# Kernel tuning notes

Hardware: AMD Instinct MI355X
Metric: run time of the kernel (lower is better)

## Reference

```python
import jax, jax.numpy as jnp
import numpy as np

ALPHA = 1.0
LAMBDA_ADV = 0.5
MARGIN = 0.5
EPS = 1e-8  # torch F.cosine_similarity eps


def setup_inputs() -> dict:
    key = jax.random.key(0)
    k1, k2, k3 = jax.random.split(key, 3)
    B, D, C = 8192, 1024, 1000
    features = jax.random.normal(k1, (B, D), dtype=jnp.float32)
    labels = jax.random.randint(k2, (B,), 0, C, dtype=jnp.int64)
    centers = jax.random.normal(k3, (C, D), dtype=jnp.float32)
    return {"features": features, "labels": labels, "centers": centers}


def reference(features, labels, centers):
    # --- intra-class term: gather centers, cosine-decayed MSE ---
    cb = centers[labels]                                   # [B, D]
    f_norm = jnp.maximum(jnp.linalg.norm(features, axis=1), EPS)   # [B]
    c_norm = jnp.maximum(jnp.linalg.norm(cb, axis=1), EPS)         # [B]
    sim = jnp.sum(features * cb, axis=1) / (f_norm * c_norm)       # [B]
    sq_err = jnp.sum((features - cb) ** 2, axis=1)                 # [B]
    intra_loss = jnp.mean(sq_err / jnp.exp(ALPHA * sim))

    # --- adversarial term: pairwise cosine sim as normalize + GEMM ---
    fhat = features / f_norm[:, None]                       # [B, D]
    sim_matrix = fhat @ fhat.T                              # [B, B]
    mask = labels[:, None] != labels[None, :]               # [B, B] bool
    hinge = jnp.where(mask, jax.nn.relu(MARGIN - sim_matrix), 0.0)
    n_pairs = jnp.maximum(jnp.sum(mask), 1).astype(hinge.dtype)
    adv_loss = jnp.sum(hinge) / n_pairs

    return intra_loss + LAMBDA_ADV * adv_loss
```

## Files before the change

### kernel.cpp

```cpp
#include <hip/hip_runtime.h>


typedef __attribute__((ext_vector_type(8))) short bf16x8;
typedef __attribute__((ext_vector_type(4))) float f32x4;

#define NROWS 8192
#define NDIM  1024
#define NCLS  1000
#define NTILE 32
#define NTRI  528

#define FHAT_OFF  0
#define INTRA_OFF 16777216
#define ADV_OFF   (INTRA_OFF + NROWS * 4)
#define HIST_OFF  (ADV_OFF + NTRI * 4)
#define WS_NEEDED (HIST_OFF + NCLS * 4)

static __device__ __forceinline__ unsigned short f2bf(float x) {
  unsigned u = __float_as_uint(x);
  u += 0x7fffu + ((u >> 16) & 1u);
  return (unsigned short)(u >> 16);
}

__global__ __launch_bounds__(256) void prep_kernel(
    const float* __restrict__ feat, const int* __restrict__ labels,
    const float* __restrict__ centers, unsigned short* __restrict__ fhat,
    float* __restrict__ intra_val, int* __restrict__ hist) {
  const int tid = threadIdx.x, wave = tid >> 6, lane = tid & 63;
  const int row = blockIdx.x * 4 + wave;

  const float4* fr = (const float4*)(feat + (size_t)row * NDIM);
  const int lab = labels[row];
  const float4* cr = (const float4*)(centers + (size_t)lab * NDIM);

  float4 f[4], c[4];
  #pragma unroll
  for (int j = 0; j < 4; ++j) { f[j] = fr[lane + j * 64]; c[j] = cr[lane + j * 64]; }

  float ff = 0.f, fc = 0.f, cc = 0.f, se = 0.f;
  #pragma unroll
  for (int j = 0; j < 4; ++j) {
    ff += f[j].x*f[j].x + f[j].y*f[j].y + f[j].z*f[j].z + f[j].w*f[j].w;
    fc += f[j].x*c[j].x + f[j].y*c[j].y + f[j].z*c[j].z + f[j].w*c[j].w;
    cc += c[j].x*c[j].x + c[j].y*c[j].y + c[j].z*c[j].z + c[j].w*c[j].w;
    float dx = f[j].x-c[j].x, dy = f[j].y-c[j].y, dz = f[j].z-c[j].z, dw = f[j].w-c[j].w;
    se += dx*dx + dy*dy + dz*dz + dw*dw;
  }

  #pragma unroll
  for (int off = 1; off < 64; off <<= 1) {
    ff += __shfl_xor(ff, off, 64);
    fc += __shfl_xor(fc, off, 64);
    cc += __shfl_xor(cc, off, 64);
    se += __shfl_xor(se, off, 64);
  }

  const float fn = fmaxf(sqrtf(ff), 1e-8f);
  const float cn = fmaxf(sqrtf(cc), 1e-8f);
  const float inv = 1.0f / fn;
  if (lane == 0) {
    intra_val[row] = se * expf(-(fc / (fn * cn)));
    atomicAdd(&hist[lab], 1);
  }

  ushort4* orow = (ushort4*)(fhat + (size_t)row * NDIM);
  #pragma unroll
  for (int j = 0; j < 4; ++j) {
    ushort4 o;
    o.x = f2bf(f[j].x * inv); o.y = f2bf(f[j].y * inv);
    o.z = f2bf(f[j].z * inv); o.w = f2bf(f[j].w * inv);
    orow[lane + j * 64] = o;
  }
}

#define CUMUL(r) ((r) * NTILE - (r) * ((r) - 1) / 2)

__global__ __launch_bounds__(512) void gemm_hinge_kernel(
    const unsigned short* __restrict__ fhat, const int* __restrict__ labels,
    float* __restrict__ adv_val) {
  const int bid0 = blockIdx.x;
  const int bid  = (bid0 & 7) * 66 + (bid0 >> 3);
  const float nf = (float)NTILE + 0.5f;
  int ti = (int)floorf(nf - sqrtf(nf * nf - 2.0f * (float)bid));
  while (ti > 0 && bid < CUMUL(ti)) --ti;
  while (bid >= CUMUL(ti + 1)) ++ti;
  const int tj = ti + (bid - CUMUL(ti));

  __shared__ __align__(16) unsigned short Al[2][256 * 32];
  __shared__ __align__(16) unsigned short Bl[2][256 * 32];
  __shared__ int labi[256], labj[256];
  __shared__ float rsum[8];

  const int tid  = threadIdx.x;
  const int wave = tid >> 6, lane = tid & 63;
  const int wr = wave >> 2, wc = wave & 3;

  if (tid < 256) labi[tid] = labels[ti * 256 + tid];
  else           labj[tid - 256] = labels[tj * 256 + (tid - 256)];

  f32x4 acc[8][4] = {};

  const int srow = tid >> 2;
  const int scol = (tid & 3) * 8;
  const unsigned short* a0 = fhat + (size_t)(ti * 256 + srow) * NDIM + scol;
  const unsigned short* b0 = fhat + (size_t)(tj * 256 + srow) * NDIM + scol;

#define STAGE(buf, k0)                                                        \
  do {                                                                        \
    _Pragma("unroll")                                                         \
    for (int l = 0; l < 2; ++l) {                                             \
      __builtin_amdgcn_global_load_lds(                                       \
          (const __attribute__((address_space(1))) void*)(a0 + (k0) +         \
              (size_t)l * 128 * NDIM),                                        \
          (__attribute__((address_space(3))) void*)&Al[buf][l * 4096 + wave * 512], \
          16, 0, 0);                                                          \
      __builtin_amdgcn_global_load_lds(                                       \
          (const __attribute__((address_space(1))) void*)(b0 + (k0) +         \
              (size_t)l * 128 * NDIM),                                        \
          (__attribute__((address_space(3))) void*)&Bl[buf][l * 4096 + wave * 512], \
          16, 0, 0);                                                          \
    }                                                                         \
  } while (0)

#define COMPUTE(buf)                                                          \
  do {                                                                        \
    const int lr = lane & 15;                                                 \
    const int lk = (lane >> 4) * 8;                                           \
    bf16x8 a[8], b[4];                                                        \
    _Pragma("unroll")                                                         \
    for (int m = 0; m < 8; ++m)                                               \
      a[m] = *(const bf16x8*)&Al[buf][(wr * 128 + m * 16 + lr) * 32 + lk];    \
    _Pragma("unroll")                                                         \
    for (int n = 0; n < 4; ++n)                                               \
      b[n] = *(const bf16x8*)&Bl[buf][(wc * 64 + n * 16 + lr) * 32 + lk];     \
    _Pragma("unroll")                                                         \
    for (int m = 0; m < 8; ++m)                                               \
      _Pragma("unroll")                                                       \
      for (int n = 0; n < 4; ++n)                                             \
        acc[m][n] = __builtin_amdgcn_mfma_f32_16x16x32_bf16(                  \
            a[m], b[n], acc[m][n], 0, 0, 0);                                  \
  } while (0)

  STAGE(0, 0);
  __syncthreads();
  for (int t = 0; t < 31; ++t) {
    const int cur = t & 1;
    STAGE(cur ^ 1, (t + 1) * 32);
    COMPUTE(cur);
    __syncthreads();
  }
  COMPUTE(1);

#undef STAGE
#undef COMPUTE

  float hs = 0.f;
  const int crow = (lane >> 4) * 4;
  const int ccol = lane & 15;
  #pragma unroll
  for (int m = 0; m < 8; ++m) {
    #pragma unroll
    for (int n = 0; n < 4; ++n) {
      #pragma unroll
      for (int r = 0; r < 4; ++r) {
        const int i = wr * 128 + m * 16 + crow + r;
        const int j = wc * 64 + n * 16 + ccol;
        if (labi[i] != labj[j]) {
          hs += fmaxf(0.5f - acc[m][n][r], 0.f);
        }
      }
    }
  }
  #pragma unroll
  for (int off = 32; off; off >>= 1) hs += __shfl_down(hs, off, 64);
  if (lane == 0) rsum[wave] = hs;
  __syncthreads();
  if (tid == 0) {
    float s = 0.f;
    #pragma unroll
    for (int w = 0; w < 8; ++w) s += rsum[w];
    if (ti != tj) s *= 2.f;
    adv_val[bid0] = s;
  }
}

__global__ __launch_bounds__(1024) void finalize_kernel(
    const float* __restrict__ intra_val, const float* __restrict__ adv_val,
    const int* __restrict__ hist, float* __restrict__ out) {
  __shared__ float rsi[16], rsa[16];
  __shared__ long long rsq[16];
  const int tid = threadIdx.x;
  const int wave = tid >> 6, lane = tid & 63;

  float si = 0.f;
  for (int i = tid; i < NROWS; i += 1024) si += intra_val[i];
  float sa = 0.f;
  if (tid < NTRI) sa = adv_val[tid];
  long long sq = 0;
  if (tid < NCLS) { long long h = hist[tid]; sq = h * h; }

  #pragma unroll
  for (int off = 32; off; off >>= 1) {
    si += __shfl_down(si, off, 64);
    sa += __shfl_down(sa, off, 64);
    sq += __shfl_down(sq, off, 64);
  }
  if (lane == 0) { rsi[wave] = si; rsa[wave] = sa; rsq[wave] = sq; }
  __syncthreads();
  if (tid == 0) {
    float SI = 0.f, SA = 0.f; long long SQ = 0;
    for (int w = 0; w < 16; ++w) { SI += rsi[w]; SA += rsa[w]; SQ += rsq[w]; }
    long long npairs = (long long)NROWS * NROWS - SQ;
    if (npairs < 1) npairs = 1;
    out[0] = SI / (float)NROWS + 0.5f * (SA / (float)npairs);
  }
}

__global__ void sentinel_kernel(float* out) {
  if (threadIdx.x == 0 && blockIdx.x == 0) out[0] = -1.0f;
}

extern "C" void kernel_launch(void* const* d_in, const int* in_sizes, int n_in,
                              void* d_out, int out_size, void* d_ws, size_t ws_size,
                              hipStream_t stream) {
  const float* feat    = (const float*)d_in[0];
  const int*   labels  = (const int*)d_in[1];
  const float* centers = (const float*)d_in[2];
  float* out = (float*)d_out;

  if (ws_size < (size_t)WS_NEEDED) {
    sentinel_kernel<<<1, 64, 0, stream>>>(out);
    return;
  }

  char* ws = (char*)d_ws;
  unsigned short* fhat = (unsigned short*)(ws + FHAT_OFF);
  float* intra_val = (float*)(ws + INTRA_OFF);
  float* adv_val   = (float*)(ws + ADV_OFF);
  int*   hist      = (int*)(ws + HIST_OFF);

  hipMemsetAsync(ws + HIST_OFF, 0, NCLS * 4, stream);

  prep_kernel<<<NROWS / 4, 256, 0, stream>>>(feat, labels, centers, fhat,
                                             intra_val, hist);
  gemm_hinge_kernel<<<NTRI, 512, 0, stream>>>(fhat, labels, adv_val);
  finalize_kernel<<<1, 1024, 0, stream>>>(intra_val, adv_val, hist, out);
}
```

Baseline: 204.9 us.

## Double K-tile to 64 with XOR-swizzled LDS and explicit waitcnt pipelining

Result: faster. 182.0 us (-11.2%).

```diff
diff --git a/kernel.cpp b/kernel.cpp
--- a/kernel.cpp
+++ b/kernel.cpp
@@ -46,7 +46,6 @@
     float dx = f[j].x-c[j].x, dy = f[j].y-c[j].y, dz = f[j].z-c[j].z, dw = f[j].w-c[j].w;
     se += dx*dx + dy*dy + dz*dz + dw*dw;
   }
-
   #pragma unroll
   for (int off = 1; off < 64; off <<= 1) {
     ff += __shfl_xor(ff, off, 64);
@@ -54,7 +53,6 @@
     cc += __shfl_xor(cc, off, 64);
     se += __shfl_xor(se, off, 64);
   }
-
   const float fn = fmaxf(sqrtf(ff), 1e-8f);
   const float cn = fmaxf(sqrtf(cc), 1e-8f);
   const float inv = 1.0f / fn;
@@ -62,7 +60,6 @@
     intra_val[row] = se * expf(-(fc / (fn * cn)));
     atomicAdd(&hist[lab], 1);
   }
-
   ushort4* orow = (ushort4*)(fhat + (size_t)row * NDIM);
   #pragma unroll
   for (int j = 0; j < 4; ++j) {
@@ -86,8 +83,8 @@
   while (bid >= CUMUL(ti + 1)) ++ti;
   const int tj = ti + (bid - CUMUL(ti));
 
-  __shared__ __align__(16) unsigned short Al[2][256 * 32];
-  __shared__ __align__(16) unsigned short Bl[2][256 * 32];
+  __shared__ __align__(16) unsigned short Al[2][256 * 64];
+  __shared__ __align__(16) unsigned short Bl[2][256 * 64];
   __shared__ int labi[256], labj[256];
   __shared__ float rsum[8];
 
@@ -100,57 +97,81 @@
 
   f32x4 acc[8][4] = {};
 
-  const int srow = tid >> 2;
-  const int scol = (tid & 3) * 8;
-  const unsigned short* a0 = fhat + (size_t)(ti * 256 + srow) * NDIM + scol;
-  const unsigned short* b0 = fhat + (size_t)(tj * 256 + srow) * NDIM + scol;
-
-#define STAGE(buf, k0)                                                        \
+  const int l8 = lane >> 3;
+  const int sl = ((lane & 7) ^ l8) * 8;
+  const unsigned short* aS = fhat + (size_t)(ti * 256 + wave * 32 + l8) * NDIM + sl;
+  const unsigned short* bS = fhat + (size_t)(tj * 256 + wave * 32 + l8) * NDIM + sl;
+
+#define STAGE(BUF, K0)                                                        \
   do {                                                                        \
     _Pragma("unroll")                                                         \
-    for (int l = 0; l < 2; ++l) {                                             \
+    for (int j = 0; j < 4; ++j) {                                             \
       __builtin_amdgcn_global_load_lds(                                       \
-          (const __attribute__((address_space(1))) void*)(a0 + (k0) +         \
-              (size_t)l * 128 * NDIM),                                        \
-          (__attribute__((address_space(3))) void*)&Al[buf][l * 4096 + wave * 512], \
+          (const __attribute__((address_space(1))) void*)(aS + (K0) + j * 8 * NDIM), \
+          (__attribute__((address_space(3))) void*)&Al[BUF][(wave * 4 + j) * 512],   \
           16, 0, 0);                                                          \
       __builtin_amdgcn_global_load_lds(                                       \
-          (const __attribute__((address_space(1))) void*)(b0 + (k0) +         \
-              (size_t)l * 128 * NDIM),                                        \
-          (__attribute__((address_space(3))) void*)&Bl[buf][l * 4096 + wave * 512], \
+          (const __attribute__((address_space(1))) void*)(bS + (K0) + j * 8 * NDIM), \
+          (__attribute__((address_space(3))) void*)&Bl[BUF][(wave * 4 + j) * 512],   \
           16, 0, 0);                                                          \
     }                                                                         \
   } while (0)
 
-#define COMPUTE(buf)                                                          \
+  const int lr = lane & 15;
+  const int hk = (lane >> 4) * 8;
+  const int xr = (lr & 7) << 3;
+
+#define COMPUTE(BUF)                                                          \
   do {                                                                        \
-    const int lr = lane & 15;                                                 \
-    const int lk = (lane >> 4) * 8;                                           \
-    bf16x8 a[8], b[4];                                                        \
     _Pragma("unroll")                                                         \
-    for (int m = 0; m < 8; ++m)                                               \
-      a[m] = *(const bf16x8*)&Al[buf][(wr * 128 + m * 16 + lr) * 32 + lk];    \
-    _Pragma("unroll")                                                         \
-    for (int n = 0; n < 4; ++n)                                               \
-      b[n] = *(const bf16x8*)&Bl[buf][(wc * 64 + n * 16 + lr) * 32 + lk];     \
-    _Pragma("unroll")                                                         \
-    for (int m = 0; m < 8; ++m)                                               \
+    for (int kk = 0; kk < 2; ++kk) {                                          \
+      const int lk = kk * 32 + hk;                                            \
+      const int lx = lk ^ xr;                                                 \
+      bf16x8 a[8], b[4];                                                      \
+      _Pragma("unroll")                                                       \
+      for (int m = 0; m < 8; ++m)                                             \
+        a[m] = *(const bf16x8*)&Al[BUF][(wr * 128 + m * 16 + lr) * 64 + lx];  \
       _Pragma("unroll")                                                       \
       for (int n = 0; n < 4; ++n)                                             \
-        acc[m][n] = __builtin_amdgcn_mfma_f32_16x16x32_bf16(                  \
-            a[m], b[n], acc[m][n], 0, 0, 0);                                  \
+        b[n] = *(const bf16x8*)&Bl[BUF][(wc * 64 + n * 16 + lr) * 64 + lx];   \
+      _Pragma("unroll")                                                       \
+      for (int m = 0; m < 8; ++m)                                             \
+        _Pragma("unroll")                                                     \
+        for (int n = 0; n < 4; ++n)                                           \
+          acc[m][n] = __builtin_amdgcn_mfma_f32_16x16x32_bf16(                \
+              a[m], b[n], acc[m][n], 0, 0, 0);                                \
+    }                                                                         \
   } while (0)
 
+#define KITER(T, CBUF)                                                        \
+  do {                                                                        \
+    STAGE(CBUF ^ 1, ((T) + 1) * 64);                                          \
+    __builtin_amdgcn_sched_barrier(0);                                        \
+    asm volatile("s_waitcnt vmcnt(8)" ::: "memory");                          \
+    __builtin_amdgcn_sched_barrier(0);                                        \
+    __builtin_amdgcn_s_barrier();                                             \
+    __builtin_amdgcn_sched_barrier(0);                                        \
+    COMPUTE(CBUF);                                                            \
+    asm volatile("s_waitcnt lgkmcnt(0)" ::: "memory");                        \
+    __builtin_amdgcn_sched_barrier(0);                                        \
+    __builtin_amdgcn_s_barrier();                                             \
+    __builtin_amdgcn_sched_barrier(0);                                        \
+  } while (0)
+
   STAGE(0, 0);
-  __syncthreads();
-  for (int t = 0; t < 31; ++t) {
-    const int cur = t & 1;
-    STAGE(cur ^ 1, (t + 1) * 32);
-    COMPUTE(cur);
-    __syncthreads();
-  }
+  #pragma unroll 1
+  for (int t2 = 0; t2 < 7; ++t2) {
+    KITER(2 * t2, 0);
+    KITER(2 * t2 + 1, 1);
+  }
+  KITER(14, 0);
+  asm volatile("s_waitcnt vmcnt(0)" ::: "memory");
+  __builtin_amdgcn_sched_barrier(0);
+  __builtin_amdgcn_s_barrier();
+  __builtin_amdgcn_sched_barrier(0);
   COMPUTE(1);
 
+#undef KITER
 #undef STAGE
 #undef COMPUTE
 
```
